# Optimization experiments

Measured on AMD Instinct MI355X. Metric: run time of the kernel, lower is better.

The kernel has to match this reference:

```python
import jax, jax.numpy as jnp
import numpy as np

# Static config derived from init_kwargs / input shapes
N, H, W, C = 4, 224, 224, 256
F = 256            # filters
K = 3              # kernel_size
BS = 16            # block_size (input block edge)
OB = BS - K + 1    # output_block_size = 14 (valid conv of a block)
STRIDE = OB        # block_stride == output_block_size
BC = 16            # block_count = divup(224, 14) = 16
PAD = K // 2       # 'same' padding -> ZeroPadding2D(1)
TOL = 0.5


def setup_inputs() -> dict:
    key = jax.random.key(0)
    k1, k2, k3, k4 = jax.random.split(key, 4)
    inputs = jax.random.normal(k1, (N, H, W, C), jnp.float32)
    mask = jax.random.uniform(k2, (N, H, W, 1), jnp.float32)
    # learned params (kernel HWIO, bias) per glorot-ish scale
    kernel = jax.random.normal(k3, (K, K, C, F), jnp.float32) * 0.02
    bias = jax.random.normal(k4, (F,), jnp.float32) * 0.01
    return {"inputs": inputs, "mask": mask, "kernel": kernel, "bias": bias}


def reference(inputs, mask, kernel, bias):
    # 'same' path: zero-pad inputs and mask (ZeroPadding2D(pad_h=1, pad_w=1))
    pi = jnp.pad(inputs, ((0, 0), (PAD, PAD), (PAD, PAD), (0, 0)))
    pm = jnp.pad(mask, ((0, 0), (PAD, PAD), (PAD, PAD), (0, 0)))

    # block gather: input blocks of size BS at stride STRIDE (overlap K-1)
    starts = jnp.arange(BC) * STRIDE                 # [BC]
    idx = starts[:, None] + jnp.arange(BS)           # [BC, BS]
    A = idx[:, None, :, None]                        # h-index -> [BC,1,BS,1]
    B = idx[None, :, None, :]                        # w-index -> [1,BC,1,BS]
    blocks = pi[:, A, B, :]                          # [N, BC, BC, BS, BS, C]
    mblocks = pm[:, A, B, :]                         # [N, BC, BC, BS, BS, 1]

    # reduce_mask with avgpool=True: block is active iff mean(mask block) > tol
    pooled = jnp.mean(mblocks, axis=(3, 4, 5))       # [N, BC, BC]
    active = (pooled > TOL).astype(inputs.dtype)     # [N, BC, BC]

    # dense VALID conv on all blocks (equiv to conv on gathered active blocks)
    x = blocks.reshape(N * BC * BC, BS, BS, C)
    y = jax.lax.conv_general_dilated(
        x, kernel, window_strides=(1, 1), padding='VALID',
        dimension_numbers=('NHWC', 'HWIO', 'NHWC'))   # [N*BC*BC, OB, OB, F]
    y = jax.nn.relu(y + bias)

    # scatter: inactive blocks remain zero; active blocks tile output exactly
    y = y.reshape(N, BC, BC, OB, OB, F) * active[:, :, :, None, None, None]
    out = y.transpose(0, 1, 3, 2, 4, 5).reshape(N, BC * OB, BC * OB, F)
    return out  # [N, 224, 224, F]
```

## Files before the change

kernel.cpp:

```cpp
#include <hip/hip_runtime.h>
#include <hip/hip_bf16.h>

#define H 224
#define W 224
#define C 256
#define F 256
#define OB 14

typedef __attribute__((ext_vector_type(8))) short short8;
typedef __attribute__((ext_vector_type(4))) float f32x4;

__device__ __forceinline__ unsigned short f2bf(float f) {
    union { float f; unsigned u; } v; v.f = f;
    unsigned r = v.u + 0x7fffu + ((v.u >> 16) & 1u);
    return (unsigned short)(r >> 16);
}

__global__ __launch_bounds__(256) void repack_kernel(const float* __restrict__ wsrc,
                                                     unsigned short* __restrict__ wrep) {
    int g = blockIdx.x * 256 + threadIdx.x;
    int lane = g & 63;
    int nt   = (g >> 6) & 15;
    int kt   = g >> 10;
    int kk   = kt >> 3, c32 = kt & 7;
    int quad = lane >> 4, lq = lane & 15;
    int cbase = c32 * 32 + quad * 8;
    int f = nt * 16 + lq;
    alignas(16) unsigned short tmp[8];
#pragma unroll
    for (int j = 0; j < 8; ++j) {
        tmp[j] = f2bf(wsrc[((size_t)(kk * 256 + cbase + j)) * 256 + f]);
    }
    *reinterpret_cast<uint4*>(wrep + (size_t)g * 8) = *reinterpret_cast<const uint4*>(tmp);
}

__global__ void init_kernel(int* __restrict__ cnt) {
    cnt[0] = 0;
    cnt[1] = 0;
}

__global__ __launch_bounds__(256) void flags_kernel(const float* __restrict__ mask,
                                                    int* __restrict__ list,
                                                    int* __restrict__ cnt) {
    int b = blockIdx.x;
    int n = b >> 8, by = (b >> 4) & 15, bx = b & 15;
    int t = threadIdx.x;
    int r = t >> 4, s = t & 15;
    int gy = by * OB - 1 + r, gx = bx * OB - 1 + s;
    float v = 0.f;
    if ((unsigned)gy < (unsigned)H && (unsigned)gx < (unsigned)W)
        v = mask[((size_t)n * H + gy) * W + gx];
    __shared__ float red[256];
    red[t] = v;
    __syncthreads();
    if (t < 64) {
        float x = red[t] + red[t + 64] + red[t + 128] + red[t + 192];
#pragma unroll
        for (int off = 32; off; off >>= 1) x += __shfl_down(x, off);
        if (t == 0) {
            if (x > 0.5f * 256.0f) {
                int p = atomicAdd(&cnt[0], 1);
                list[p] = b;
            } else {
                int p = atomicAdd(&cnt[1], 1);
                list[1023 - p] = b;
            }
        }
    }
}

__global__ __launch_bounds__(512, 2) void conv_kernel(const float* __restrict__ in,
                                                      const unsigned short* __restrict__ wrep,
                                                      const float* __restrict__ bias,
                                                      const int* __restrict__ list,
                                                      const int* __restrict__ cnt,
                                                      float* __restrict__ out) {
    __shared__ __align__(16) unsigned short patch[256 * 128];

    const int bid = blockIdx.x;
    const int n_active = cnt[0];
    const int b = list[bid];
    const int n = b >> 8, by = (b >> 4) & 15, bx = b & 15;
    const int tid = threadIdx.x;
    const int gy0 = by * OB - 1, gx0 = bx * OB - 1;
    float* outB = out + (size_t)n * H * W * F;

    if (bid >= n_active) {
#pragma unroll 4
        for (int idx = tid; idx < 196 * 64; idx += 512) {
            int pix = idx >> 6, fv = idx & 63;
            int oy = pix / 14, ox = pix - oy * 14;
            size_t o = ((size_t)((by * OB + oy) * W + bx * OB + ox)) * F + fv * 4;
            *reinterpret_cast<float4*>(outB + o) = make_float4(0.f, 0.f, 0.f, 0.f);
        }
        return;
    }

    const int wave = tid >> 6, lane = tid & 63;
    const int quad = lane >> 4, lq = lane & 15;
    const int wm = wave >> 2;
    const int wn = wave & 3;

    f32x4 acc[7][4];
#pragma unroll
    for (int r = 0; r < 7; ++r)
#pragma unroll
        for (int i = 0; i < 4; ++i) acc[r][i] = (f32x4)(0.f);

    const float* inB = in + (size_t)n * H * W * C;
    const int scol_base = (lq > 13) ? 13 : lq;
    const unsigned short* wrep_w = wrep + ((size_t)(wn * 4) * 64 + lane) * 8;

    for (int cc = 0; cc < 2; ++cc) {
        __syncthreads();
#pragma unroll 4
        for (int it = 0; it < 16; ++it) {
            int idx = tid + it * 512;
            int pix = idx >> 5, chv = idx & 31;
            int r = pix >> 4, s = pix & 15;
            int gy = gy0 + r, gx = gx0 + s;
            float4 v = make_float4(0.f, 0.f, 0.f, 0.f);
            if ((unsigned)gy < (unsigned)H && (unsigned)gx < (unsigned)W)
                v = *reinterpret_cast<const float4*>(inB + ((size_t)(gy * W + gx)) * C + cc * 128 + chv * 4);
            uint2 bb;
            bb.x = (unsigned)f2bf(v.x) | ((unsigned)f2bf(v.y) << 16);
            bb.y = (unsigned)f2bf(v.z) | ((unsigned)f2bf(v.w) << 16);
            int g = chv >> 1, hh = chv & 1;
            int soff = (pix << 7) + ((g ^ (pix & 15)) << 3) + (hh << 2);
            *reinterpret_cast<uint2*>(&patch[soff]) = bb;
        }
        __syncthreads();

#pragma unroll 1
        for (int ky = 0; ky < 3; ++ky) {
#pragma unroll 1
            for (int kx = 0; kx < 3; ++kx) {
                const int kk = ky * 3 + kx;
                const int scol = scol_base + kx;
                const unsigned short* bp = wrep_w + (size_t)(kk * 8 + cc * 4) * 8192;
                const int sb = (((wm * 7 + ky) << 4) + scol) << 7;
#pragma unroll 2
                for (int c32l = 0; c32l < 4; ++c32l) {
                    const unsigned short* bpc = bp + c32l * 8192;
                    short8 b0 = *reinterpret_cast<const short8*>(bpc);
                    short8 b1 = *reinterpret_cast<const short8*>(bpc + 512);
                    short8 b2 = *reinterpret_cast<const short8*>(bpc + 1024);
                    short8 b3 = *reinterpret_cast<const short8*>(bpc + 1536);
                    const int gq = (c32l << 2) + quad;
                    const unsigned short* ap = &patch[sb + ((gq ^ scol) << 3)];
#pragma unroll
                    for (int r = 0; r < 7; ++r) {
                        short8 a = *reinterpret_cast<const short8*>(ap + r * 2048);
                        acc[r][0] = __builtin_amdgcn_mfma_f32_16x16x32_bf16(a, b0, acc[r][0], 0, 0, 0);
                        acc[r][1] = __builtin_amdgcn_mfma_f32_16x16x32_bf16(a, b1, acc[r][1], 0, 0, 0);
                        acc[r][2] = __builtin_amdgcn_mfma_f32_16x16x32_bf16(a, b2, acc[r][2], 0, 0, 0);
                        acc[r][3] = __builtin_amdgcn_mfma_f32_16x16x32_bf16(a, b3, acc[r][3], 0, 0, 0);
                    }
                }
            }
        }
    }

    float bv[4];
#pragma unroll
    for (int i = 0; i < 4; ++i) bv[i] = bias[wn * 64 + i * 16 + lq];
#pragma unroll
    for (int r = 0; r < 7; ++r) {
        const int oy = wm * 7 + r;
#pragma unroll
        for (int j = 0; j < 4; ++j) {
            const int ox = quad * 4 + j;
            if (ox < 14) {
                size_t o = ((size_t)((by * OB + oy) * W + bx * OB + ox)) * F + wn * 64 + lq;
#pragma unroll
                for (int i = 0; i < 4; ++i) {
                    float v = acc[r][i][j] + bv[i];
                    outB[o + i * 16] = v > 0.f ? v : 0.f;
                }
            }
        }
    }
}

extern "C" void kernel_launch(void* const* d_in, const int* in_sizes, int n_in,
                              void* d_out, int out_size, void* d_ws, size_t ws_size,
                              hipStream_t stream) {
    const float* inputs = (const float*)d_in[0];
    const float* mask   = (const float*)d_in[1];
    const float* wsrc   = (const float*)d_in[2];
    const float* bias   = (const float*)d_in[3];
    float* outp = (float*)d_out;

    unsigned short* wrep = (unsigned short*)d_ws;
    int* list = (int*)((char*)d_ws + 1179648);
    int* cnt  = (int*)((char*)d_ws + 1179648 + 4096);

    hipLaunchKernelGGL(init_kernel, dim3(1), dim3(1), 0, stream, cnt);
    hipLaunchKernelGGL(repack_kernel, dim3(288), dim3(256), 0, stream, wsrc, wrep);
    hipLaunchKernelGGL(flags_kernel, dim3(1024), dim3(256), 0, stream, mask, list, cnt);
    hipLaunchKernelGGL(conv_kernel, dim3(1024), dim3(512), 0, stream,
                       inputs, wrep, bias, list, cnt, outp);
}
```

Baseline: 434.0 us.

## Double-buffer input patch across channel chunks and double conv block threads

Measured after the change: 429.7 us. Within noise of the previous version (-1.0%).

```diff
diff --git a/kernel.cpp b/kernel.cpp
--- a/kernel.cpp
+++ b/kernel.cpp
@@ -69,13 +69,13 @@
     }
 }
 
-__global__ __launch_bounds__(512, 2) void conv_kernel(const float* __restrict__ in,
-                                                      const unsigned short* __restrict__ wrep,
-                                                      const float* __restrict__ bias,
-                                                      const int* __restrict__ list,
-                                                      const int* __restrict__ cnt,
-                                                      float* __restrict__ out) {
-    __shared__ __align__(16) unsigned short patch[256 * 128];
+__global__ __launch_bounds__(1024, 4) void conv_kernel(const float* __restrict__ in,
+                                                       const unsigned short* __restrict__ wrep,
+                                                       const float* __restrict__ bias,
+                                                       const int* __restrict__ list,
+                                                       const int* __restrict__ cnt,
+                                                       float* __restrict__ out) {
+    __shared__ __align__(16) unsigned short patch[2][256 * 64];
 
     const int bid = blockIdx.x;
     const int n_active = cnt[0];
@@ -87,7 +87,7 @@
 
     if (bid >= n_active) {
 #pragma unroll 4
-        for (int idx = tid; idx < 196 * 64; idx += 512) {
+        for (int idx = tid; idx < 196 * 64; idx += 1024) {
             int pix = idx >> 6, fv = idx & 63;
             int oy = pix / 14, ox = pix - oy * 14;
             size_t o = ((size_t)((by * OB + oy) * W + bx * OB + ox)) * F + fv * 4;
@@ -98,72 +98,107 @@
 
     const int wave = tid >> 6, lane = tid & 63;
     const int quad = lane >> 4, lq = lane & 15;
-    const int wm = wave >> 2;
-    const int wn = wave & 3;
-
-    f32x4 acc[7][4];
-#pragma unroll
-    for (int r = 0; r < 7; ++r)
-#pragma unroll
-        for (int i = 0; i < 4; ++i) acc[r][i] = (f32x4)(0.f);
+    const int wm = wave >> 3;
+    const int wn = wave & 7;
 
     const float* inB = in + (size_t)n * H * W * C;
+
+    const float* sp[4];
+    int so[4];
+#pragma unroll
+    for (int it = 0; it < 4; ++it) {
+        int idx = tid + (it << 10);
+        int pix = idx >> 4, chv = idx & 15;
+        int rr = pix >> 4, ss = pix & 15;
+        int gy = gy0 + rr, gx = gx0 + ss;
+        bool ok = ((unsigned)gy < (unsigned)H) && ((unsigned)gx < (unsigned)W);
+        sp[it] = ok ? (inB + ((size_t)(gy * W + gx)) * C + chv * 4) : nullptr;
+        so[it] = (pix << 6) + (((chv >> 1) ^ (pix & 7)) << 3) + ((chv & 1) << 2);
+    }
+
+    f32x4 acc[7][2];
+#pragma unroll
+    for (int r = 0; r < 7; ++r) {
+        acc[r][0] = (f32x4)(0.f);
+        acc[r][1] = (f32x4)(0.f);
+    }
+
     const int scol_base = (lq > 13) ? 13 : lq;
-    const unsigned short* wrep_w = wrep + ((size_t)(wn * 4) * 64 + lane) * 8;
-
-    for (int cc = 0; cc < 2; ++cc) {
-        __syncthreads();
-#pragma unroll 4
-        for (int it = 0; it < 16; ++it) {
-            int idx = tid + it * 512;
-            int pix = idx >> 5, chv = idx & 31;
-            int r = pix >> 4, s = pix & 15;
-            int gy = gy0 + r, gx = gx0 + s;
-            float4 v = make_float4(0.f, 0.f, 0.f, 0.f);
-            if ((unsigned)gy < (unsigned)H && (unsigned)gx < (unsigned)W)
-                v = *reinterpret_cast<const float4*>(inB + ((size_t)(gy * W + gx)) * C + cc * 128 + chv * 4);
-            uint2 bb;
-            bb.x = (unsigned)f2bf(v.x) | ((unsigned)f2bf(v.y) << 16);
-            bb.y = (unsigned)f2bf(v.z) | ((unsigned)f2bf(v.w) << 16);
-            int g = chv >> 1, hh = chv & 1;
-            int soff = (pix << 7) + ((g ^ (pix & 15)) << 3) + (hh << 2);
-            *reinterpret_cast<uint2*>(&patch[soff]) = bb;
-        }
-        __syncthreads();
-
+    const unsigned short* wb = wrep + ((size_t)(wn * 2) * 64 + lane) * 8;
+    const int arow_base = (wm * 7 * 16) << 6;
+
+#pragma unroll
+    for (int it = 0; it < 4; ++it) {
+        float4 v = make_float4(0.f, 0.f, 0.f, 0.f);
+        if (sp[it]) v = *reinterpret_cast<const float4*>(sp[it]);
+        uint2 bb;
+        bb.x = (unsigned)f2bf(v.x) | ((unsigned)f2bf(v.y) << 16);
+        bb.y = (unsigned)f2bf(v.z) | ((unsigned)f2bf(v.w) << 16);
+        *reinterpret_cast<uint2*>(&patch[0][so[it]]) = bb;
+    }
+    __syncthreads();
+
+    int cur = 0;
 #pragma unroll 1
-        for (int ky = 0; ky < 3; ++ky) {
+    for (int cc = 0; cc < 4; ++cc) {
+        const bool pf = (cc < 3);
+        float4 st[4];
+        if (pf) {
+#pragma unroll
+            for (int it = 0; it < 4; ++it) {
+                st[it] = make_float4(0.f, 0.f, 0.f, 0.f);
+                if (sp[it]) st[it] = *reinterpret_cast<const float4*>(sp[it] + (cc + 1) * 64);
+            }
+        }
+        const unsigned short* pc = &patch[cur][0];
 #pragma unroll 1
-            for (int kx = 0; kx < 3; ++kx) {
-                const int kk = ky * 3 + kx;
-                const int scol = scol_base + kx;
-                const unsigned short* bp = wrep_w + (size_t)(kk * 8 + cc * 4) * 8192;
-                const int sb = (((wm * 7 + ky) << 4) + scol) << 7;
-#pragma unroll 2
-                for (int c32l = 0; c32l < 4; ++c32l) {
-                    const unsigned short* bpc = bp + c32l * 8192;
-                    short8 b0 = *reinterpret_cast<const short8*>(bpc);
-                    short8 b1 = *reinterpret_cast<const short8*>(bpc + 512);
-                    short8 b2 = *reinterpret_cast<const short8*>(bpc + 1024);
-                    short8 b3 = *reinterpret_cast<const short8*>(bpc + 1536);
-                    const int gq = (c32l << 2) + quad;
-                    const unsigned short* ap = &patch[sb + ((gq ^ scol) << 3)];
-#pragma unroll
-                    for (int r = 0; r < 7; ++r) {
-                        short8 a = *reinterpret_cast<const short8*>(ap + r * 2048);
-                        acc[r][0] = __builtin_amdgcn_mfma_f32_16x16x32_bf16(a, b0, acc[r][0], 0, 0, 0);
-                        acc[r][1] = __builtin_amdgcn_mfma_f32_16x16x32_bf16(a, b1, acc[r][1], 0, 0, 0);
-                        acc[r][2] = __builtin_amdgcn_mfma_f32_16x16x32_bf16(a, b2, acc[r][2], 0, 0, 0);
-                        acc[r][3] = __builtin_amdgcn_mfma_f32_16x16x32_bf16(a, b3, acc[r][3], 0, 0, 0);
+        for (int kx = 0; kx < 3; ++kx) {
+            const int scol = scol_base + kx;
+            const int sw = scol & 7;
+            const int acol = arow_base + (scol << 6);
+#pragma unroll 1
+            for (int c32l = 0; c32l < 2; ++c32l) {
+                const unsigned short* ap = pc + acol + ((((c32l << 2) + quad) ^ sw) << 3);
+                const unsigned short* wbk = wb + (cc * 2 + c32l) * 8192 + kx * 65536;
+                short8 bf[3][2];
+#pragma unroll
+                for (int ky = 0; ky < 3; ++ky) {
+                    bf[ky][0] = *reinterpret_cast<const short8*>(wbk + ky * 196608);
+                    bf[ky][1] = *reinterpret_cast<const short8*>(wbk + ky * 196608 + 512);
+                }
+                __builtin_amdgcn_s_setprio(1);
+#pragma unroll
+                for (int rowl = 0; rowl < 9; ++rowl) {
+                    short8 a = *reinterpret_cast<const short8*>(ap + (rowl << 10));
+#pragma unroll
+                    for (int ky = 0; ky < 3; ++ky) {
+                        const int r = rowl - ky;
+                        if (r >= 0 && r < 7) {
+                            acc[r][0] = __builtin_amdgcn_mfma_f32_16x16x32_bf16(a, bf[ky][0], acc[r][0], 0, 0, 0);
+                            acc[r][1] = __builtin_amdgcn_mfma_f32_16x16x32_bf16(a, bf[ky][1], acc[r][1], 0, 0, 0);
+                        }
                     }
                 }
-            }
-        }
-    }
-
-    float bv[4];
-#pragma unroll
-    for (int i = 0; i < 4; ++i) bv[i] = bias[wn * 64 + i * 16 + lq];
+                __builtin_amdgcn_s_setprio(0);
+            }
+            if (kx == 0 && pf) {
+#pragma unroll
+                for (int it = 0; it < 4; ++it) {
+                    uint2 bb;
+                    bb.x = (unsigned)f2bf(st[it].x) | ((unsigned)f2bf(st[it].y) << 16);
+                    bb.y = (unsigned)f2bf(st[it].z) | ((unsigned)f2bf(st[it].w) << 16);
+                    *reinterpret_cast<uint2*>(&patch[cur ^ 1][so[it]]) = bb;
+                }
+            }
+        }
+        if (pf) {
+            __syncthreads();
+            cur ^= 1;
+        }
+    }
+
+    const float bv0 = bias[wn * 32 + lq];
+    const float bv1 = bias[wn * 32 + 16 + lq];
 #pragma unroll
     for (int r = 0; r < 7; ++r) {
         const int oy = wm * 7 + r;
@@ -171,12 +206,11 @@
         for (int j = 0; j < 4; ++j) {
             const int ox = quad * 4 + j;
             if (ox < 14) {
-                size_t o = ((size_t)((by * OB + oy) * W + bx * OB + ox)) * F + wn * 64 + lq;
-#pragma unroll
-                for (int i = 0; i < 4; ++i) {
-                    float v = acc[r][i][j] + bv[i];
-                    outB[o + i * 16] = v > 0.f ? v : 0.f;
-                }
+                size_t o = ((size_t)((by * OB + oy) * W + bx * OB + ox)) * F + wn * 32 + lq;
+                float v0 = acc[r][0][j] + bv0;
+                float v1 = acc[r][1][j] + bv1;
+                outB[o]      = v0 > 0.f ? v0 : 0.f;
+                outB[o + 16] = v1 > 0.f ? v1 : 0.f;
             }
         }
     }
@@ -198,6 +232,6 @@
     hipLaunchKernelGGL(init_kernel, dim3(1), dim3(1), 0, stream, cnt);
     hipLaunchKernelGGL(repack_kernel, dim3(288), dim3(256), 0, stream, wsrc, wrep);
     hipLaunchKernelGGL(flags_kernel, dim3(1024), dim3(256), 0, stream, mask, list, cnt);
-    hipLaunchKernelGGL(conv_kernel, dim3(1024), dim3(512), 0, stream,
+    hipLaunchKernelGGL(conv_kernel, dim3(1024), dim3(1024), 0, stream,
                        inputs, wrep, bias, list, cnt, outp);
 }
```
